# Kernel optimization log

Hardware: AMD Instinct MI355X
Metric: run time of the kernel (lower is better)

## Reference

```python
import jax, jax.numpy as jnp
from jax import lax
import numpy as np
import math

# --- static equivariant-conv basis (kernel lattice offsets) ---
K = 5          # kernel size = diameter / step
NRB = 3        # num_radial_basis
RMAX = 2.5     # diameter / 2
C0, C1 = 32, 16   # hidden irreps: 32x0e + 16x1e (4*ne scalars + 2*ne vectors, ne=8)
GATES = C1        # one 0e gate scalar per gated vector irrep

_c = np.arange(K, dtype=np.float32) - K // 2
_grid = np.stack(np.meshgrid(_c, _c, _c, indexing='ij'), -1)            # [K,K,K,3]
_norm = np.linalg.norm(_grid, axis=-1)
_mask = (_norm <= RMAX).astype(np.float32)
_ctr = np.linspace(0.0, RMAX, NRB).astype(np.float32)
_w = RMAX / (NRB - 1)
R_BASIS = jnp.asarray(np.exp(-(((_norm[..., None] - _ctr) / _w) ** 2)) * _mask[..., None])  # [K,K,K,NRB]
_safe = np.where(_norm == 0.0, 1.0, _norm)
_y1 = (math.sqrt(3.0) * _grid / _safe[..., None]).astype(np.float32)    # component-normalized l=1 SH
_y1[_norm == 0.0] = 0.0
Y1_SH = jnp.asarray(_y1)                                                # [K,K,K,3]
_levi = np.zeros((3, 3, 3), np.float32)
for _a, _b, _d in ((0, 1, 2), (1, 2, 0), (2, 0, 1)):
    _levi[_a, _b, _d] = 1.0
    _levi[_a, _d, _b] = -1.0
LEVI = jnp.asarray(_levi)


def _equiv_conv(x, ss, sv, vs, vv0, vv1):
    """Equivariant voxel conv: kernel = radial(|r|) * Y_l(r) * CG, then 3D conv.
    x: [B,D,H,W, C0 + 3*C1] -> [B,D,H,W, Cso + 3*Cvo]."""
    Cso, Cvo = ss.shape[-1], sv.shape[-1]
    Kss = jnp.einsum('xyzr,rio->xyzio', R_BASIS, ss)                      # 0e->0e via Y0
    Ksv = jnp.einsum('xyzr,rio,xyzm->xyziom', R_BASIS, sv, Y1_SH)         # 0e->1  via Y1
    Kvs = jnp.einsum('xyzr,rio,xyzm->xyzimo', R_BASIS, vs, Y1_SH) / math.sqrt(3.0)  # 1->0 (dot CG)
    Kvv0 = jnp.einsum('xyzr,rio->xyzio', R_BASIS, vv0)                    # 1->1 via Y0 (identity CG)
    Kvv1 = jnp.einsum('xyzr,rio->xyzio', R_BASIS, vv1)                    # 1->1 via Y1 (cross CG)
    E1 = jnp.einsum('xyzm,amb->xyzab', Y1_SH, LEVI) / math.sqrt(2.0)
    eye = jnp.eye(3, dtype=x.dtype)
    Kvv = (Kvv0[..., :, None, :, None] * eye[None, None, None, None, :, None, :]
           + Kvv1[..., :, None, :, None] * E1[..., None, :, None, :])     # [K,K,K,C1,3,Cvo,3]
    top = jnp.concatenate([Kss, Ksv.reshape(K, K, K, C0, 3 * Cvo)], axis=-1)
    bot = jnp.concatenate([Kvs.reshape(K, K, K, 3 * C1, Cso),
                           Kvv.reshape(K, K, K, 3 * C1, 3 * Cvo)], axis=-1)
    kern = jnp.concatenate([top, bot], axis=-2)                            # [K,K,K,Fin,Fout]
    return lax.conv_general_dilated(x, kern, (1, 1, 1), 'SAME',
                                    dimension_numbers=('NDHWC', 'DHWIO', 'NDHWC'))


def _gate(y):
    """e3nn Gate: activation on scalars, sigmoid(gates) scales the vectors."""
    s = jax.nn.relu(y[..., :C0])
    g = jax.nn.sigmoid(y[..., C0:C0 + GATES])
    v = y[..., C0 + GATES:].reshape(y.shape[:-1] + (C1, 3)) * g[..., None]
    return jnp.concatenate([s, v.reshape(y.shape[:-1] + (3 * C1,))], axis=-1)


def _up2(a, axes=(1, 2, 3)):
    for ax in axes:
        a = jnp.repeat(a, 2, axis=ax)
    return a


def _forward(x, c1_ss, c1_sv, c1_vs, c1_vv0, c1_vv1,
             c2_ss, c2_sv, c2_vs, c2_vv0, c2_vv1, w_pos, wl_s, wl_v):
    # --- ConvolutionBlock: two equivariant convs, each followed by a Gate ---
    x = _gate(_equiv_conv(x, c1_ss, c1_sv, c1_vs, c1_vv0, c1_vv1))
    x = _gate(_equiv_conv(x, c2_ss, c2_sv, c2_vs, c2_vv0, c2_vv1))
    B, Dc, Hc, Wc, _F = x.shape
    # --- _get_vectors: fine-grid offsets to (recentered) upsampled coarse centers ---
    ci = jnp.stack(jnp.meshgrid(jnp.arange(Dc), jnp.arange(Hc), jnp.arange(Wc), indexing='ij'), -1)
    centers = _up2((ci + jnp.array([Dc // 2, Hc // 2, Wc // 2]))[None], (1, 2, 3))[0].astype(jnp.float32)
    fi = jnp.stack(jnp.meshgrid(jnp.arange(2 * Dc), jnp.arange(2 * Hc), jnp.arange(2 * Wc),
                                indexing='ij'), -1).astype(jnp.float32)
    vecs = fi - centers                               # [2D,2H,2W,3]
    p = w_pos * vecs                                  # position_blocks: irreps-wise 1x1 Linear
    # --- nearest-neighbor upsample of features ---
    xu = _up2(x)                                      # [B,2D,2H,2W,F]
    S = xu[..., :C0]
    V = xu[..., C0:].reshape(xu.shape[:-1] + (C1, 3))
    # --- FullTensorProduct(features, pos embedding): per-voxel CG contractions ---
    t_s = jnp.einsum('bxyzcm,xyzm->bxyzc', V, p) / math.sqrt(3.0)          # 1x1->0
    t_v_sp = S[..., None] * p[None, :, :, :, None, :]                       # 0x1->1
    t_v_vp = jnp.cross(V, p[None, :, :, :, None, :]) / math.sqrt(2.0)       # 1x1->1
    tv = jnp.concatenate([t_v_sp, t_v_vp], axis=-2)                         # [...,C0+C1,3]
    # --- rebase_blocks_linear: irreps-wise Linear back to hidden (fan-in normalized) ---
    S_out = jnp.einsum('bxyzc,co->bxyzo', t_s, wl_s) / math.sqrt(C1)
    V_out = jnp.einsum('bxyzcm,co->bxyzom', tv, wl_v) / math.sqrt(C0 + C1)
    return jnp.concatenate([S_out, V_out.reshape(V_out.shape[:-2] + (3 * C1,))], axis=-1)


def setup_inputs() -> dict:
    key = jax.random.key(0)
    ks = jax.random.split(key, 16)
    n = jax.random.normal
    s = 0.02
    B, D = 1, 32
    FIN = C0 + 3 * C1          # 80
    CSO = C0 + GATES           # 48 output scalars (incl. gates) per conv
    return {
        'x': n(ks[0], (B, D, D, D, FIN), jnp.float32),
        'c1_ss': s * n(ks[1], (NRB, C0, CSO), jnp.float32),
        'c1_sv': s * n(ks[2], (NRB, C0, C1), jnp.float32),
        'c1_vs': s * n(ks[3], (NRB, C1, CSO), jnp.float32),
        'c1_vv0': s * n(ks[4], (NRB, C1, C1), jnp.float32),
        'c1_vv1': s * n(ks[5], (NRB, C1, C1), jnp.float32),
        'c2_ss': s * n(ks[6], (NRB, C0, CSO), jnp.float32),
        'c2_sv': s * n(ks[7], (NRB, C0, C1), jnp.float32),
        'c2_vs': s * n(ks[8], (NRB, C1, CSO), jnp.float32),
        'c2_vv0': s * n(ks[9], (NRB, C1, C1), jnp.float32),
        'c2_vv1': s * n(ks[10], (NRB, C1, C1), jnp.float32),
        'w_pos': 0.1 * n(ks[11], (), jnp.float32),
        'wl_s': n(ks[12], (C1, C0), jnp.float32),
        'wl_v': n(ks[13], (C0 + C1, C1), jnp.float32),
    }


def reference(x, c1_ss, c1_sv, c1_vs, c1_vv0, c1_vv1,
              c2_ss, c2_sv, c2_vs, c2_vv0, c2_vv1, w_pos, wl_s, wl_v):
    return _forward(x, c1_ss, c1_sv, c1_vs, c1_vv0, c1_vv1,
                    c2_ss, c2_sv, c2_vs, c2_vv0, c2_vv1, w_pos, wl_s, wl_v)
```

## Files before the change

kernel.cpp:

```cpp
#include <hip/hip_runtime.h>
#include <math.h>


typedef __attribute__((ext_vector_type(8))) short bf16x8;
typedef __attribute__((ext_vector_type(4))) float f32x4;

__device__ __forceinline__ int eps3(int a, int m, int b) {
    if (a == b || a == m || m == b) return 0;
    return ((a==0&&m==1&&b==2)||(a==1&&m==2&&b==0)||(a==2&&m==0&&b==1)) ? 1 : -1;
}

struct TapTab {
    int   op[40];
    float R[40][3];
    float RY[40][9];
    float Rc[3];
};
constexpr float cexpf_(float x) {
    float y = x * (1.f/16.f);
    float s = 1.f + y*(1.f + y*(0.5f + y*((1.f/6.f) + y*((1.f/24.f) + y*(1.f/120.f)))));
    s *= s; s *= s; s *= s; s *= s;
    return s;
}
constexpr float csqrtf_(float x) {
    float g = x > 1.f ? x : 1.f;
    for (int i = 0; i < 40; i++) g = 0.5f*(g + x/g);
    return g;
}
constexpr TapTab make_taps() {
    TapTab T{};
    int idx = 0;
    for (int t = 0; t < 125; t++) {
        int td = t/25 - 2, th = (t/5)%5 - 2, tw = t%5 - 2;
        int n2 = td*td + th*th + tw*tw;
        if (t == 62) {
            for (int r = 0; r < 3; r++) {
                float tt = (0.f - 1.25f*(float)r) * 0.8f;
                T.Rc[r] = cexpf_(-tt*tt);
            }
            continue;
        }
        bool active = n2 <= 6;
        bool pos = (td>0) || (td==0 && th>0) || (td==0 && th==0 && tw>0);
        if (!(active && pos)) continue;
        T.op[idx] = (td*96 + th*12 + tw) * 18;
        float norm = csqrtf_((float)n2);
        float comp[3] = {(float)td, (float)th, (float)tw};
        for (int r = 0; r < 3; r++) {
            float tt = (norm - 1.25f*(float)r) * 0.8f;
            float R = cexpf_(-tt*tt);
            T.R[idx][r] = R;
            for (int m = 0; m < 3; m++)
                T.RY[idx][r*3+m] = R * 1.7320508075688772f * comp[m] / norm;
        }
        idx++;
    }
    return T;
}
__device__ constexpr TapTab TT = make_taps();

__global__ void build_W(float* __restrict__ W,
    const float* __restrict__ ss1, const float* __restrict__ sv1,
    const float* __restrict__ vs1, const float* __restrict__ vv01, const float* __restrict__ vv11,
    const float* __restrict__ ss2, const float* __restrict__ sv2,
    const float* __restrict__ vs2, const float* __restrict__ vv02, const float* __restrict__ vv12)
{
    int idx = threadIdx.x + blockIdx.x * 256;
    if (idx >= 184320) return;
    int conv = idx / 92160;
    int rem  = idx % 92160;
    int j  = rem / 7680;
    int ci = (rem / 96) % 80;
    int co = rem % 96;
    int r = j >> 2, al = j & 3;
    const float* ss  = conv ? ss2  : ss1;
    const float* sv  = conv ? sv2  : sv1;
    const float* vs  = conv ? vs2  : vs1;
    const float* vv0 = conv ? vv02 : vv01;
    const float* vv1 = conv ? vv12 : vv11;
    float val = 0.f;
    if (ci < 32) {
        if (co < 48) { if (al == 0) val = ss[(r*32 + ci)*48 + co]; }
        else {
            int o = (co - 48) / 3, m = (co - 48) % 3;
            if (al == m + 1) val = sv[(r*32 + ci)*16 + o];
        }
    } else {
        int i = (ci - 32) / 3, a = (ci - 32) % 3;
        if (co < 48) { if (al == a + 1) val = vs[(r*16 + i)*48 + co] * 0.5773502691896258f; }
        else {
            int o = (co - 48) / 3, b = (co - 48) % 3;
            if (al == 0) { if (a == b) val = vv0[(r*16 + i)*16 + o]; }
            else {
                int e = eps3(a, al - 1, b);
                if (e) val = vv1[(r*16 + i)*16 + o] * (float)e * 0.7071067811865476f;
            }
        }
    }
    W[idx] = val;
}

__global__ void build_Wc(const float* __restrict__ W,
                         unsigned short* __restrict__ Wh, unsigned short* __restrict__ Wl)
{
    int idx = threadIdx.x + blockIdx.x * 256;
    if (idx >= 184320) return;
    int conv = idx / 92160, rem = idx % 92160;
    int co = rem / 960, kp = rem % 960;
    int c5 = kp / 192, r2 = kp % 192;
    int j = r2 / 16, ci16 = r2 % 16;
    int k = j * 80 + c5 * 16 + ci16;
    float w = W[conv * 92160 + k * 96 + co];
    unsigned int u = __float_as_uint(w);
    unsigned int hib = (u + 0x7FFFu + ((u >> 16) & 1u)) & 0xFFFF0000u;
    float res = w - __uint_as_float(hib);
    unsigned int v = __float_as_uint(res);
    unsigned int lob = (v + 0x7FFFu + ((v >> 16) & 1u)) >> 16;
    Wh[idx] = (unsigned short)(hib >> 16);
    Wl[idx] = (unsigned short)lob;
}


__device__ __forceinline__ void stageA(
    const float* __restrict__ smem, unsigned short* __restrict__ zch,
    unsigned short* __restrict__ zcl, int vox, int cg)
{
    int pos = ((vox >> 5) + 2) * 96 + ((((vox >> 3) & 3)) + 2) * 12 + (vox & 7) + 2;
    const float* xpb = smem + pos * 18 + 2 * cg - 3924;
    float az[12][2];
    #pragma unroll
    for (int j = 0; j < 12; j++) { az[j][0] = 0.f; az[j][1] = 0.f; }
    {
        float2 xc = *reinterpret_cast<const float2*>(xpb + 3924);
        #pragma unroll
        for (int r = 0; r < 3; r++) {
            float R = TT.Rc[r];
            az[r*4][0] += R * xc.x; az[r*4][1] += R * xc.y;
        }
    }
    #pragma unroll
    for (int p = 0; p < 40; p++) {
        float2 xa = *reinterpret_cast<const float2*>(xpb + (3924 + TT.op[p]));
        float2 xb = *reinterpret_cast<const float2*>(xpb + (3924 - TT.op[p]));
        float s0 = xa.x + xb.x, s1 = xa.y + xb.y;
        float d0 = xa.x - xb.x, d1 = xa.y - xb.y;
        #pragma unroll
        for (int r = 0; r < 3; r++) {
            float R = TT.R[p][r];
            az[r*4][0] += R * s0; az[r*4][1] += R * s1;
            #pragma unroll
            for (int m = 0; m < 3; m++) {
                float RY = TT.RY[p][r*3+m];
                az[r*4 + m + 1][0] += RY * d0;
                az[r*4 + m + 1][1] += RY * d1;
            }
        }
    }
    int swz = (vox >> 3) & 3;
    int cg3 = cg & 3;
    #pragma unroll
    for (int j = 0; j < 12; j++) {
        unsigned int hw = 0, lw = 0;
        #pragma unroll
        for (int e = 0; e < 2; e++) {
            float a = az[j][e];
            unsigned int u = __float_as_uint(a);
            unsigned int hi = u >> 16;
            float res = a - __uint_as_float(u & 0xFFFF0000u);
            unsigned int lo2 = __float_as_uint(res) >> 16;
            hw |= hi << (16 * e);
            lw |= lo2 << (16 * e);
        }
        int k = j * 16 + 2 * cg;
        int g = k >> 3;
        int blk = g >> 2, sub = (g & 3) ^ swz;
        int offu = vox * 200 + blk * 32 + sub * 8 + 2 * cg3;
        *reinterpret_cast<unsigned int*>(zch + offu) = hw;
        *reinterpret_cast<unsigned int*>(zcl + offu) = lw;
    }
}

__device__ __forceinline__ void stageB(
    const unsigned short* __restrict__ zch, const unsigned short* __restrict__ zcl,
    const unsigned short* __restrict__ Wh, const unsigned short* __restrict__ Wl,
    int c, int brow, int bnh, int lr, int lk, f32x4* acc)
{
    int swzB = (brow >> 3) & 3;
    const unsigned short* zh = zch + brow * 200;
    const unsigned short* zl = zcl + brow * 200;
    const unsigned short* wb  = Wh + (bnh * 48 + lr) * 960 + c * 192 + lk * 8;
    const unsigned short* wbl = Wl + (bnh * 48 + lr) * 960 + c * 192 + lk * 8;
    int sub = (lk ^ swzB) * 8;
    #pragma unroll
    for (int ks = 0; ks < 6; ks++) {
        bf16x8 bh[3], bl[3];
        #pragma unroll
        for (int nt = 0; nt < 3; nt++) {
            bh[nt] = *reinterpret_cast<const bf16x8*>(wb  + nt * 15360 + ks * 32);
            bl[nt] = *reinterpret_cast<const bf16x8*>(wbl + nt * 15360 + ks * 32);
        }
        int ao = ks * 32 + sub;
        bf16x8 ah = *reinterpret_cast<const bf16x8*>(zh + ao);
        bf16x8 al = *reinterpret_cast<const bf16x8*>(zl + ao);
        #pragma unroll
        for (int nt = 0; nt < 3; nt++) {
            acc[nt] = __builtin_amdgcn_mfma_f32_16x16x32_bf16(ah, bh[nt], acc[nt], 0, 0, 0);
            acc[nt] = __builtin_amdgcn_mfma_f32_16x16x32_bf16(al, bh[nt], acc[nt], 0, 0, 0);
            acc[nt] = __builtin_amdgcn_mfma_f32_16x16x32_bf16(ah, bl[nt], acc[nt], 0, 0, 0);
        }
    }
}

__global__ __attribute__((amdgpu_flat_work_group_size(1024, 1024), amdgpu_waves_per_eu(4)))
void fused_conv(
    const float* __restrict__ xin, const unsigned short* __restrict__ Wh,
    const unsigned short* __restrict__ Wl, float* __restrict__ xout)
{
    __shared__ float smem[39424];
    unsigned short* zch = reinterpret_cast<unsigned short*>(smem + 13824);
    unsigned short* zcl = reinterpret_cast<unsigned short*>(smem + 26624);
    int tid = threadIdx.x;
    int wv = tid >> 6, l = tid & 63;
    int lr = l & 15, lk = l >> 4;
    bool logrp = wv < 8;
    int cg = wv & 7;
    int brt = (wv & 7) >> 1, bnh = wv & 1;
    int rowbase = (logrp ? 0 : 64) + brt * 16;
    int brow = rowbase + lr;
    int bid = blockIdx.x;
    int dt = (bid >> 5) << 2;
    int h0 = ((bid >> 2) & 7) << 2;
    int w0 = (bid & 3) << 3;

    int gof[3], lof[3];
    #pragma unroll
    for (int q = 0; q < 3; q++) {
        int i = tid + q * 1024;
        int sl = i / 768, rr = i - sl * 768;
        int dd = rr / 96, rm = rr - dd * 96;
        int hh = rm / 12, ww = rm - hh * 12;
        int gd = dt + dd - 2, gh = h0 + hh - 2, gw = w0 + ww - 2;
        gof[q] = (gd >= 0 && gd < 32 && gh >= 0 && gh < 32 && gw >= 0 && gw < 32)
               ? (((gd << 5) + gh) * 32 + gw) * 80 + sl * 4 : -1;
        lof[q] = rr * 18 + sl * 4;
    }

    {
        float4 pf[3];
        #pragma unroll
        for (int q = 0; q < 3; q++)
            pf[q] = (gof[q] >= 0) ? *reinterpret_cast<const float4*>(xin + gof[q])
                                  : make_float4(0.f, 0.f, 0.f, 0.f);
        #pragma unroll
        for (int q = 0; q < 3; q++) {
            *reinterpret_cast<float2*>(smem + lof[q])     = make_float2(pf[q].x, pf[q].y);
            *reinterpret_cast<float2*>(smem + lof[q] + 2) = make_float2(pf[q].z, pf[q].w);
        }
    }
    __syncthreads();

    const f32x4 fzero = {0.f, 0.f, 0.f, 0.f};
    f32x4 acc[3];
    #pragma unroll
    for (int nt = 0; nt < 3; nt++) acc[nt] = fzero;

    for (int c = 0; c < 5; c++) {
        float4 pf[3];
        if (c < 4) {
            int chof = (c + 1) * 16;
            #pragma unroll
            for (int q = 0; q < 3; q++)
                pf[q] = (gof[q] >= 0) ? *reinterpret_cast<const float4*>(xin + gof[q] + chof)
                                      : make_float4(0.f, 0.f, 0.f, 0.f);
        }
        if (logrp)      stageA(smem, zch, zcl, l, cg);
        else if (c > 0) stageB(zch, zcl, Wh, Wl, c - 1, brow, bnh, lr, lk, acc);
        __syncthreads();
        if (logrp) stageB(zch, zcl, Wh, Wl, c, brow, bnh, lr, lk, acc);
        else       stageA(smem, zch, zcl, 64 + l, cg);
        __syncthreads();
        if (c < 4) {
            #pragma unroll
            for (int q = 0; q < 3; q++) {
                *reinterpret_cast<float2*>(smem + lof[q])     = make_float2(pf[q].x, pf[q].y);
                *reinterpret_cast<float2*>(smem + lof[q] + 2) = make_float2(pf[q].z, pf[q].w);
            }
        }
        __syncthreads();
    }
    if (!logrp) stageB(zch, zcl, Wh, Wl, 4, brow, bnh, lr, lk, acc);
    __syncthreads();

    float* y = smem;
    #pragma unroll
    for (int nt = 0; nt < 3; nt++)
        #pragma unroll
        for (int r = 0; r < 4; r++)
            y[(rowbase + lk * 4 + r) * 98 + bnh * 48 + nt * 16 + lr] = acc[nt][r];
    __syncthreads();
    #pragma unroll
    for (int it = 0; it < 10; it++) {
        int idx = tid + it * 1024;
        int vr = idx / 80, c = idx - vr * 80;
        int gd = dt + (vr >> 5), gh = h0 + ((vr >> 3) & 3), gw = w0 + (vr & 7);
        const float* yr = y + vr * 98;
        float val;
        if (c < 32) val = fmaxf(yr[c], 0.f);
        else {
            int q = c - 32;
            float g = 1.f / (1.f + __expf(-yr[32 + q / 3]));
            val = yr[48 + q] * g;
        }
        xout[(size_t)(((gd << 5) + gh) * 32 + gw) * 80 + c] = val;
    }
}

__global__ __launch_bounds__(256) void final_k(
    const float* __restrict__ x2, const float* __restrict__ wls,
    const float* __restrict__ wlv, const float* __restrict__ wpos,
    float* __restrict__ out)
{
    __shared__ float xv[16 * 81];
    __shared__ float coeff[16 * 161];
    __shared__ float s_wls[512];
    __shared__ float s_wlv[768];
    int t = threadIdx.x;
    int bid = blockIdx.x;
    int cw0 = (bid & 1) * 16;
    int ch  = (bid >> 1) & 31;
    int cd  = bid >> 6;
    float wp = wpos[0];
    {
        int base = ((cd * 32 + ch) * 32 + cw0) * 80;
        #pragma unroll
        for (int i = t; i < 1280; i += 256) {
            int vi = i / 80, c = i % 80;
            xv[vi * 81 + c] = x2[base + i];
        }
        for (int i = t; i < 512; i += 256) s_wls[i] = wls[i];
        for (int i = t; i < 768; i += 256) s_wlv[i] = wlv[i];
    }
    __syncthreads();
    {
        int vi = t >> 4, j = t & 15;
        const float* xp = xv + vi * 81;
        float* cf = coeff + vi * 161;
        #pragma unroll
        for (int l = 0; l < 10; l++) {
            int q = l * 16 + j;
            float sum = 0.f;
            if (q < 96) {
                int o = q / 3, m = q % 3;
                #pragma unroll
                for (int c = 0; c < 16; c++) sum += xp[32 + c * 3 + m] * s_wls[c * 32 + o];
            } else if (q < 112) {
                int o = q - 96;
                #pragma unroll
                for (int c = 0; c < 32; c++) sum += xp[c] * s_wlv[c * 16 + o];
            } else {
                int q2 = q - 112; int o = q2 / 3, m = q2 % 3;
                #pragma unroll
                for (int c = 0; c < 16; c++) sum += xp[32 + c * 3 + m] * s_wlv[(32 + c) * 16 + o];
            }
            cf[q] = sum;
        }
    }
    __syncthreads();
    const float scale = 0.14433756729740643f;
    #pragma unroll
    for (int f01 = 0; f01 < 4; f01++) {
        int fd = 2 * cd + (f01 >> 1), fh = 2 * ch + (f01 & 1);
        float p0 = wp * (float)(cd + (f01 >> 1) - 16);
        float p1 = wp * (float)(ch + (f01 & 1) - 16);
        size_t obase = (size_t)((fd * 64 + fh) * 64 + cw0 * 2) * 80;
        #pragma unroll
        for (int it = 0; it < 3; it++) {
            int idx4 = it * 256 + t;
            if (idx4 < 640) {
                int base = idx4 * 4;
                int fwl = base / 80, c0 = base - fwl * 80;
                int vi = fwl >> 1;
                float p2 = wp * (float)(cw0 + vi + (fwl & 1) - 16);
                const float* cf = coeff + vi * 161;
                float vv[4];
                if (c0 < 32) {
                    #pragma unroll
                    for (int e = 0; e < 4; e++) {
                        int c = c0 + e;
                        vv[e] = cf[c * 3] * p0 + cf[c * 3 + 1] * p1 + cf[c * 3 + 2] * p2;
                    }
                } else {
                    #pragma unroll
                    for (int e = 0; e < 4; e++) {
                        int q = c0 - 32 + e, o = q / 3, m = q - o * 3;
                        float A = cf[96 + o];
                        const float* w2 = cf + 112 + o * 3;
                        float pm, crm;
                        if (m == 0)      { pm = p0; crm = w2[1] * p2 - w2[2] * p1; }
                        else if (m == 1) { pm = p1; crm = w2[2] * p0 - w2[0] * p2; }
                        else             { pm = p2; crm = w2[0] * p1 - w2[1] * p0; }
                        vv[e] = A * pm + crm * 0.7071067811865476f;
                    }
                }
                f32x4 o4 = {vv[0]*scale, vv[1]*scale, vv[2]*scale, vv[3]*scale};
                __builtin_nontemporal_store(o4, reinterpret_cast<f32x4*>(out + obase + base));
            }
        }
    }
}

extern "C" void kernel_launch(void* const* d_in, const int* in_sizes, int n_in,
                              void* d_out, int out_size, void* d_ws, size_t ws_size,
                              hipStream_t stream)
{
    const float* x    = (const float*)d_in[0];
    const float* wpos = (const float*)d_in[11];
    const float* wls  = (const float*)d_in[12];
    const float* wlv  = (const float*)d_in[13];
    float* out = (float*)d_out;
    float* ws  = (float*)d_ws;

    float* W   = ws + 1024;
    unsigned short* Wh = (unsigned short*)(ws + 1024 + 184320);
    unsigned short* Wl = Wh + 184320;
    float* x1  = ws + 1024 + 184320 + 184320;
    float* x2  = x1 + 2621440;

    build_W<<<720, 256, 0, stream>>>(W,
        (const float*)d_in[1], (const float*)d_in[2], (const float*)d_in[3],
        (const float*)d_in[4], (const float*)d_in[5],
        (const float*)d_in[6], (const float*)d_in[7], (const float*)d_in[8],
        (const float*)d_in[9], (const float*)d_in[10]);
    build_Wc<<<720, 256, 0, stream>>>(W, Wh, Wl);

    fused_conv<<<256, 1024, 0, stream>>>(x,  Wh,         Wl,         x1);
    fused_conv<<<256, 1024, 0, stream>>>(x1, Wh + 92160, Wl + 92160, x2);
    final_k<<<2048, 256, 0, stream>>>(x2, wls, wlv, wpos, out);
}
```

Baseline: 358.2 us.

## Split fused conv into producer/consumer waves with double-buffered smaller tiles

Restructures the fused conv kernel from 1024-thread blocks of 128 voxels into 512-thread blocks of 64 voxels. Four waves only build the radial/SH tap projections and the other four only run MFMA and prefetch the next channel slice. The projected activations are double-buffered in shared memory, and channel chunks drop to 8 so the halo tile is smaller. The weight packing layout is reordered to match, and each MFMA wave now covers all 96 outputs. The goal is to overlap the VALU-heavy tap stage with the MFMA stage and raise occupancy through lower LDS use, at the cost of more channel iterations and barriers.

```diff
diff --git a/kernel.cpp b/kernel.cpp
--- a/kernel.cpp
+++ b/kernel.cpp
@@ -4,6 +4,7 @@
 
 typedef __attribute__((ext_vector_type(8))) short bf16x8;
 typedef __attribute__((ext_vector_type(4))) float f32x4;
+typedef __attribute__((ext_vector_type(4))) unsigned int u32x4;
 
 __device__ __forceinline__ int eps3(int a, int m, int b) {
     if (a == b || a == m || m == b) return 0;
@@ -43,7 +44,7 @@
         bool active = n2 <= 6;
         bool pos = (td>0) || (td==0 && th>0) || (td==0 && th==0 && tw>0);
         if (!(active && pos)) continue;
-        T.op[idx] = (td*96 + th*12 + tw) * 18;
+        T.op[idx] = (td*96 + th*12 + tw) * 10;
         float norm = csqrtf_((float)n2);
         float comp[3] = {(float)td, (float)th, (float)tw};
         for (int r = 0; r < 3; r++) {
@@ -107,9 +108,11 @@
     if (idx >= 184320) return;
     int conv = idx / 92160, rem = idx % 92160;
     int co = rem / 960, kp = rem % 960;
-    int c5 = kp / 192, r2 = kp % 192;
-    int j = r2 / 16, ci16 = r2 % 16;
-    int k = j * 80 + c5 * 16 + ci16;
+    int c10 = kp / 96, r2 = kp % 96;
+    int cg = r2 / 24, r3 = r2 % 24;
+    int e = r3 / 12, j = r3 % 12;
+    int ci = c10 * 8 + cg * 2 + e;
+    int k = j * 80 + ci;
     float w = W[conv * 92160 + k * 96 + co];
     unsigned int u = __float_as_uint(w);
     unsigned int hib = (u + 0x7FFFu + ((u >> 16) & 1u)) & 0xFFFF0000u;
@@ -121,17 +124,27 @@
 }
 
 
+__device__ __forceinline__ void halo_slot(int i, int dt, int h0, int w0, int& go, int& lo) {
+    int pos = i >> 1, half = i & 1;
+    int hd = pos / 96, rm = pos - hd * 96;
+    int hh = rm / 12, hw = rm - hh * 12;
+    int gd = dt + hd - 2, gh = h0 + hh - 2, gw = w0 + hw - 2;
+    go = (gd >= 0 && gd < 32 && gh >= 0 && gh < 32 && gw >= 0 && gw < 32)
+       ? (((gd << 5) + gh) * 32 + gw) * 80 + half * 4 : -1;
+    lo = pos * 10 + half * 4;
+}
+
 __device__ __forceinline__ void stageA(
     const float* __restrict__ smem, unsigned short* __restrict__ zch,
     unsigned short* __restrict__ zcl, int vox, int cg)
 {
-    int pos = ((vox >> 5) + 2) * 96 + ((((vox >> 3) & 3)) + 2) * 12 + (vox & 7) + 2;
-    const float* xpb = smem + pos * 18 + 2 * cg - 3924;
+    int pos = ((vox >> 5) + 2) * 96 + (((vox >> 3) & 3) + 2) * 12 + (vox & 7) + 2;
+    const float* xpb = smem + pos * 10 + 2 * cg - 2180;
     float az[12][2];
     #pragma unroll
     for (int j = 0; j < 12; j++) { az[j][0] = 0.f; az[j][1] = 0.f; }
     {
-        float2 xc = *reinterpret_cast<const float2*>(xpb + 3924);
+        float2 xc = *reinterpret_cast<const float2*>(xpb + 2180);
         #pragma unroll
         for (int r = 0; r < 3; r++) {
             float R = TT.Rc[r];
@@ -140,8 +153,8 @@
     }
     #pragma unroll
     for (int p = 0; p < 40; p++) {
-        float2 xa = *reinterpret_cast<const float2*>(xpb + (3924 + TT.op[p]));
-        float2 xb = *reinterpret_cast<const float2*>(xpb + (3924 - TT.op[p]));
+        float2 xa = *reinterpret_cast<const float2*>(xpb + (2180 + TT.op[p]));
+        float2 xb = *reinterpret_cast<const float2*>(xpb + (2180 - TT.op[p]));
         float s0 = xa.x + xb.x, s1 = xa.y + xb.y;
         float d0 = xa.x - xb.x, d1 = xa.y - xb.y;
         #pragma unroll
@@ -156,151 +169,139 @@
             }
         }
     }
-    int swz = (vox >> 3) & 3;
-    int cg3 = cg & 3;
-    #pragma unroll
-    for (int j = 0; j < 12; j++) {
-        unsigned int hw = 0, lw = 0;
-        #pragma unroll
-        for (int e = 0; e < 2; e++) {
-            float a = az[j][e];
-            unsigned int u = __float_as_uint(a);
-            unsigned int hi = u >> 16;
-            float res = a - __uint_as_float(u & 0xFFFF0000u);
-            unsigned int lo2 = __float_as_uint(res) >> 16;
-            hw |= hi << (16 * e);
-            lw |= lo2 << (16 * e);
-        }
-        int k = j * 16 + 2 * cg;
-        int g = k >> 3;
-        int blk = g >> 2, sub = (g & 3) ^ swz;
-        int offu = vox * 200 + blk * 32 + sub * 8 + 2 * cg3;
-        *reinterpret_cast<unsigned int*>(zch + offu) = hw;
-        *reinterpret_cast<unsigned int*>(zcl + offu) = lw;
-    }
+    unsigned int uh[12], ul[12];
+    #pragma unroll
+    for (int e = 0; e < 2; e++)
+        #pragma unroll
+        for (int j2 = 0; j2 < 6; j2++) {
+            float a0 = az[2*j2][e], a1 = az[2*j2+1][e];
+            unsigned int b0 = __float_as_uint(a0), b1 = __float_as_uint(a1);
+            float r0 = a0 - __uint_as_float(b0 & 0xFFFF0000u);
+            float r1 = a1 - __uint_as_float(b1 & 0xFFFF0000u);
+            uh[e*6 + j2] = (b0 >> 16) | ((b1 >> 16) << 16);
+            ul[e*6 + j2] = (__float_as_uint(r0) >> 16) | ((__float_as_uint(r1) >> 16) << 16);
+        }
+    int base = vox * 104 + cg * 24;
+    *reinterpret_cast<u32x4*>(zch + base)      = (u32x4){uh[0], uh[1], uh[2],  uh[3]};
+    *reinterpret_cast<u32x4*>(zch + base + 8)  = (u32x4){uh[4], uh[5], uh[6],  uh[7]};
+    *reinterpret_cast<u32x4*>(zch + base + 16) = (u32x4){uh[8], uh[9], uh[10], uh[11]};
+    *reinterpret_cast<u32x4*>(zcl + base)      = (u32x4){ul[0], ul[1], ul[2],  ul[3]};
+    *reinterpret_cast<u32x4*>(zcl + base + 8)  = (u32x4){ul[4], ul[5], ul[6],  ul[7]};
+    *reinterpret_cast<u32x4*>(zcl + base + 16) = (u32x4){ul[8], ul[9], ul[10], ul[11]};
 }
 
 __device__ __forceinline__ void stageB(
     const unsigned short* __restrict__ zch, const unsigned short* __restrict__ zcl,
     const unsigned short* __restrict__ Wh, const unsigned short* __restrict__ Wl,
-    int c, int brow, int bnh, int lr, int lk, f32x4* acc)
-{
-    int swzB = (brow >> 3) & 3;
-    const unsigned short* zh = zch + brow * 200;
-    const unsigned short* zl = zcl + brow * 200;
-    const unsigned short* wb  = Wh + (bnh * 48 + lr) * 960 + c * 192 + lk * 8;
-    const unsigned short* wbl = Wl + (bnh * 48 + lr) * 960 + c * 192 + lk * 8;
-    int sub = (lk ^ swzB) * 8;
-    #pragma unroll
-    for (int ks = 0; ks < 6; ks++) {
-        bf16x8 bh[3], bl[3];
-        #pragma unroll
-        for (int nt = 0; nt < 3; nt++) {
-            bh[nt] = *reinterpret_cast<const bf16x8*>(wb  + nt * 15360 + ks * 32);
-            bl[nt] = *reinterpret_cast<const bf16x8*>(wbl + nt * 15360 + ks * 32);
-        }
-        int ao = ks * 32 + sub;
-        bf16x8 ah = *reinterpret_cast<const bf16x8*>(zh + ao);
-        bf16x8 al = *reinterpret_cast<const bf16x8*>(zl + ao);
-        #pragma unroll
-        for (int nt = 0; nt < 3; nt++) {
-            acc[nt] = __builtin_amdgcn_mfma_f32_16x16x32_bf16(ah, bh[nt], acc[nt], 0, 0, 0);
-            acc[nt] = __builtin_amdgcn_mfma_f32_16x16x32_bf16(al, bh[nt], acc[nt], 0, 0, 0);
-            acc[nt] = __builtin_amdgcn_mfma_f32_16x16x32_bf16(ah, bl[nt], acc[nt], 0, 0, 0);
-        }
-    }
-}
-
-__global__ __attribute__((amdgpu_flat_work_group_size(1024, 1024), amdgpu_waves_per_eu(4)))
+    int c10, int brow, int lr, int lk, f32x4* acc)
+{
+    const unsigned short* zh = zch + brow * 104 + lk * 8;
+    const unsigned short* zl = zcl + brow * 104 + lk * 8;
+    const unsigned short* wb  = Wh + lr * 960 + c10 * 96 + lk * 8;
+    const unsigned short* wbl = Wl + lr * 960 + c10 * 96 + lk * 8;
+    #pragma unroll
+    for (int ks = 0; ks < 3; ks++) {
+        bf16x8 ah = *reinterpret_cast<const bf16x8*>(zh + ks * 32);
+        bf16x8 al = *reinterpret_cast<const bf16x8*>(zl + ks * 32);
+        #pragma unroll
+        for (int nt = 0; nt < 6; nt++) {
+            bf16x8 bh = *reinterpret_cast<const bf16x8*>(wb  + nt * 15360 + ks * 32);
+            bf16x8 bl = *reinterpret_cast<const bf16x8*>(wbl + nt * 15360 + ks * 32);
+            acc[nt] = __builtin_amdgcn_mfma_f32_16x16x32_bf16(ah, bh, acc[nt], 0, 0, 0);
+            acc[nt] = __builtin_amdgcn_mfma_f32_16x16x32_bf16(al, bh, acc[nt], 0, 0, 0);
+            acc[nt] = __builtin_amdgcn_mfma_f32_16x16x32_bf16(ah, bl, acc[nt], 0, 0, 0);
+        }
+    }
+}
+
+__global__ __attribute__((amdgpu_flat_work_group_size(512, 512), amdgpu_waves_per_eu(4)))
 void fused_conv(
     const float* __restrict__ xin, const unsigned short* __restrict__ Wh,
     const unsigned short* __restrict__ Wl, float* __restrict__ xout)
 {
-    __shared__ float smem[39424];
-    unsigned short* zch = reinterpret_cast<unsigned short*>(smem + 13824);
-    unsigned short* zcl = reinterpret_cast<unsigned short*>(smem + 26624);
-    int tid = threadIdx.x;
-    int wv = tid >> 6, l = tid & 63;
+    __shared__ float smem[19072];
+    unsigned short* zc = reinterpret_cast<unsigned short*>(smem + 5760);
+    int t = threadIdx.x;
+    int wv = t >> 6, l = t & 63;
+    bool Aw = wv < 4;
+    int vox = t & 63, cg = wv & 3;
     int lr = l & 15, lk = l >> 4;
-    bool logrp = wv < 8;
-    int cg = wv & 7;
-    int brt = (wv & 7) >> 1, bnh = wv & 1;
-    int rowbase = (logrp ? 0 : 64) + brt * 16;
+    int rowbase = (wv & 3) * 16;
     int brow = rowbase + lr;
     int bid = blockIdx.x;
-    int dt = (bid >> 5) << 2;
+    int dt = (bid >> 5) << 1;
     int h0 = ((bid >> 2) & 7) << 2;
     int w0 = (bid & 3) << 3;
 
-    int gof[3], lof[3];
+    int go5[5], lo5[5];
+    if (!Aw) {
+        #pragma unroll
+        for (int q = 0; q < 5; q++) {
+            int i = (t - 256) + q * 256;
+            if (i < 1152) halo_slot(i, dt, h0, w0, go5[q], lo5[q]);
+            else { go5[q] = -2; lo5[q] = 0; }
+        }
+    }
+
     #pragma unroll
     for (int q = 0; q < 3; q++) {
-        int i = tid + q * 1024;
-        int sl = i / 768, rr = i - sl * 768;
-        int dd = rr / 96, rm = rr - dd * 96;
-        int hh = rm / 12, ww = rm - hh * 12;
-        int gd = dt + dd - 2, gh = h0 + hh - 2, gw = w0 + ww - 2;
-        gof[q] = (gd >= 0 && gd < 32 && gh >= 0 && gh < 32 && gw >= 0 && gw < 32)
-               ? (((gd << 5) + gh) * 32 + gw) * 80 + sl * 4 : -1;
-        lof[q] = rr * 18 + sl * 4;
-    }
-
-    {
-        float4 pf[3];
-        #pragma unroll
-        for (int q = 0; q < 3; q++)
-            pf[q] = (gof[q] >= 0) ? *reinterpret_cast<const float4*>(xin + gof[q])
-                                  : make_float4(0.f, 0.f, 0.f, 0.f);
-        #pragma unroll
-        for (int q = 0; q < 3; q++) {
-            *reinterpret_cast<float2*>(smem + lof[q])     = make_float2(pf[q].x, pf[q].y);
-            *reinterpret_cast<float2*>(smem + lof[q] + 2) = make_float2(pf[q].z, pf[q].w);
+        int i = t + q * 512;
+        if (i < 1152) {
+            int go, lo; halo_slot(i, dt, h0, w0, go, lo);
+            float4 v = (go >= 0) ? *reinterpret_cast<const float4*>(xin + go)
+                                 : make_float4(0.f, 0.f, 0.f, 0.f);
+            *reinterpret_cast<float4*>(smem + lo) = v;
         }
     }
     __syncthreads();
 
     const f32x4 fzero = {0.f, 0.f, 0.f, 0.f};
-    f32x4 acc[3];
-    #pragma unroll
-    for (int nt = 0; nt < 3; nt++) acc[nt] = fzero;
-
-    for (int c = 0; c < 5; c++) {
-        float4 pf[3];
-        if (c < 4) {
-            int chof = (c + 1) * 16;
+    f32x4 acc[6];
+    #pragma unroll
+    for (int nt = 0; nt < 6; nt++) acc[nt] = fzero;
+
+    for (int c = 0; c < 10; c++) {
+        float4 pf[5];
+        if (!Aw && c < 9) {
             #pragma unroll
-            for (int q = 0; q < 3; q++)
-                pf[q] = (gof[q] >= 0) ? *reinterpret_cast<const float4*>(xin + gof[q] + chof)
-                                      : make_float4(0.f, 0.f, 0.f, 0.f);
-        }
-        if (logrp)      stageA(smem, zch, zcl, l, cg);
-        else if (c > 0) stageB(zch, zcl, Wh, Wl, c - 1, brow, bnh, lr, lk, acc);
+            for (int q = 0; q < 5; q++)
+                if (go5[q] != -2)
+                    pf[q] = (go5[q] >= 0)
+                          ? *reinterpret_cast<const float4*>(xin + go5[q] + (c + 1) * 8)
+                          : make_float4(0.f, 0.f, 0.f, 0.f);
+        }
+        unsigned short* zb = zc + (c & 1) * 13312;
+        if (Aw) stageA(smem, zb, zb + 6656, vox, cg);
+        else if (c > 0) {
+            const unsigned short* rb = zc + ((c - 1) & 1) * 13312;
+            stageB(rb, rb + 6656, Wh, Wl, c - 1, brow, lr, lk, acc);
+        }
         __syncthreads();
-        if (logrp) stageB(zch, zcl, Wh, Wl, c, brow, bnh, lr, lk, acc);
-        else       stageA(smem, zch, zcl, 64 + l, cg);
+        if (!Aw && c < 9) {
+            #pragma unroll
+            for (int q = 0; q < 5; q++)
+                if (go5[q] != -2) *reinterpret_cast<float4*>(smem + lo5[q]) = pf[q];
+        }
         __syncthreads();
-        if (c < 4) {
+    }
+    if (!Aw) {
+        const unsigned short* rb = zc + 13312;
+        stageB(rb, rb + 6656, Wh, Wl, 9, brow, lr, lk, acc);
+    }
+    __syncthreads();
+
+    float* y = smem;
+    if (!Aw) {
+        #pragma unroll
+        for (int nt = 0; nt < 6; nt++)
             #pragma unroll
-            for (int q = 0; q < 3; q++) {
-                *reinterpret_cast<float2*>(smem + lof[q])     = make_float2(pf[q].x, pf[q].y);
-                *reinterpret_cast<float2*>(smem + lof[q] + 2) = make_float2(pf[q].z, pf[q].w);
-            }
-        }
-        __syncthreads();
-    }
-    if (!logrp) stageB(zch, zcl, Wh, Wl, 4, brow, bnh, lr, lk, acc);
+            for (int r = 0; r < 4; r++)
+                y[(rowbase + lk * 4 + r) * 98 + nt * 16 + lr] = acc[nt][r];
+    }
     __syncthreads();
-
-    float* y = smem;
-    #pragma unroll
-    for (int nt = 0; nt < 3; nt++)
-        #pragma unroll
-        for (int r = 0; r < 4; r++)
-            y[(rowbase + lk * 4 + r) * 98 + bnh * 48 + nt * 16 + lr] = acc[nt][r];
-    __syncthreads();
     #pragma unroll
     for (int it = 0; it < 10; it++) {
-        int idx = tid + it * 1024;
+        int idx = t + it * 512;
         int vr = idx / 80, c = idx - vr * 80;
         int gd = dt + (vr >> 5), gh = h0 + ((vr >> 3) & 3), gw = w0 + (vr & 7);
         const float* yr = y + vr * 98;
@@ -433,7 +434,7 @@
         (const float*)d_in[9], (const float*)d_in[10]);
     build_Wc<<<720, 256, 0, stream>>>(W, Wh, Wl);
 
-    fused_conv<<<256, 1024, 0, stream>>>(x,  Wh,         Wl,         x1);
-    fused_conv<<<256, 1024, 0, stream>>>(x1, Wh + 92160, Wl + 92160, x2);
+    fused_conv<<<512, 512, 0, stream>>>(x,  Wh,         Wl,         x1);
+    fused_conv<<<512, 512, 0, stream>>>(x1, Wh + 92160, Wl + 92160, x2);
     final_k<<<2048, 256, 0, stream>>>(x2, wls, wlv, wpos, out);
 }
```

After: 617.2 us. 1.72x slower.
